# Optimization experiments

Measured on AMD Instinct MI355X. Metric: run time of the kernel, lower is better.

## Reference

```python
import jax, jax.numpy as jnp
import numpy as np

N_NODES = 10000
N_EDGES = 320000
NEG_SLOPE = 0.2
EPS = 1e-12


def _gat_layer(x, W, a_src, a_dst, b, src, dst, n, heads, out_c):
    # x: [n, in_c]; W: [in_c, heads*out_c]; a_src/a_dst: [heads, out_c]; b: [heads*out_c]
    h = (x @ W).reshape(n, heads, out_c)                     # [n, H, C]
    e_src = jnp.einsum('nhc,hc->nh', h, a_src)               # [n, H]
    e_dst = jnp.einsum('nhc,hc->nh', h, a_dst)               # [n, H]
    e = e_src[src] + e_dst[dst]                              # [E, H]
    e = jnp.where(e > 0, e, NEG_SLOPE * e)                   # leaky_relu
    # segment softmax over incoming edges of each destination node
    emax = jax.ops.segment_max(e, dst, num_segments=n)       # [n, H]
    ex = jnp.exp(e - emax[dst])                              # [E, H]
    denom = jax.ops.segment_sum(ex, dst, num_segments=n)     # [n, H]
    alpha = ex / denom[dst]                                  # [E, H]
    out = jax.ops.segment_sum(alpha[:, :, None] * h[src], dst, num_segments=n)
    return out.reshape(n, heads * out_c) + b


def setup_inputs() -> dict:
    key = jax.random.key(0)
    ks = jax.random.split(key, 16)
    n, e = N_NODES, N_EDGES
    x1 = jax.random.normal(ks[0], (n, 10), dtype=jnp.float32)
    x2 = jax.random.normal(ks[1], (n, 10), dtype=jnp.float32)
    edge_index = jax.random.randint(ks[2], (2, e), 0, n, dtype=jnp.int64)
    s = 0.2
    params = {
        'W1': jax.random.normal(ks[3], (10, 32), dtype=jnp.float32) * s,
        'a_src1': jax.random.normal(ks[4], (8, 4), dtype=jnp.float32) * s,
        'a_dst1': jax.random.normal(ks[5], (8, 4), dtype=jnp.float32) * s,
        'b1': jnp.zeros((32,), dtype=jnp.float32),
        'W2': jax.random.normal(ks[6], (32, 16), dtype=jnp.float32) * s,
        'a_src2': jax.random.normal(ks[7], (4, 4), dtype=jnp.float32) * s,
        'a_dst2': jax.random.normal(ks[8], (4, 4), dtype=jnp.float32) * s,
        'b2': jnp.zeros((16,), dtype=jnp.float32),
        'W3': jax.random.normal(ks[9], (16, 8), dtype=jnp.float32) * s,
        'a_src3': jax.random.normal(ks[10], (2, 4), dtype=jnp.float32) * s,
        'a_dst3': jax.random.normal(ks[11], (2, 4), dtype=jnp.float32) * s,
        'b3': jnp.zeros((8,), dtype=jnp.float32),
        'lin2_w': jax.random.normal(ks[12], (8, 1), dtype=jnp.float32) * s,
    }
    return {'x1': x1, 'x2': x2, 'edge_index': edge_index, 'num_nodes': n, **params}


def reference(x1, x2, edge_index, num_nodes, W1, a_src1, a_dst1, b1, W2, a_src2, a_dst2, b2, W3, a_src3, a_dst3, b3, lin2_w):
    n = num_nodes
    row, col = edge_index[0], edge_index[1]
    # dense adjacency with ones on edges, diag filled with 1, then L1 row-normalized
    adj = jnp.zeros((n, n), dtype=x1.dtype).at[row, col].set(1.0)
    diag = jnp.arange(n)
    adj = adj.at[diag, diag].set(1.0)
    adj = adj / jnp.maximum(jnp.sum(jnp.abs(adj), axis=1, keepdims=True), EPS)
    # GATConv adds self-loops internally
    sl = jnp.arange(n, dtype=edge_index.dtype)
    src = jnp.concatenate([row, sl])
    dst = jnp.concatenate([col, sl])
    x3 = jax.nn.relu(_gat_layer(x1, W1, a_src1, a_dst1, b1, src, dst, n, 8, 4))
    x4 = jax.nn.relu(_gat_layer(x3, W2, a_src2, a_dst2, b2, src, dst, n, 4, 4))
    x6 = jax.nn.relu(_gat_layer(x4, W3, a_src3, a_dst3, b3, src, dst, n, 2, 4))
    # eval mode: F.dropout is a no-op
    R = x6 @ x6.T                                            # [n, n]
    R_2 = jnp.sum(R * adj, axis=1, keepdims=True)            # [n, 1]
    local_score = R_2 + x1[:, 0:1]
    global_score = (adj @ x6) @ lin2_w                       # [n, 1]
    return local_score + global_score
```

## Files before the change

### kernel.cpp

```cpp
#include <hip/hip_runtime.h>

#define TPB 256
#define CAP 128
#define POI 0xAAAAAAAAu

__global__ __launch_bounds__(256) void scatter_t1_kernel(
        const int* __restrict__ edge, int E, int n,
        int* __restrict__ fill,  int* __restrict__ csr,
        int* __restrict__ rfill, int* __restrict__ rcsr,
        const float* __restrict__ x, const float* __restrict__ W,
        const float* __restrict__ asrc, const float* __restrict__ adst,
        float* __restrict__ h, float* __restrict__ es, float* __restrict__ ed) {
    constexpr int IN = 10, H = 8, HC = 32;
    __shared__ float sW[IN * HC];
    __shared__ float sa[HC];
    __shared__ float sd[HC];
    for (int i = threadIdx.x; i < IN * HC; i += blockDim.x) sW[i] = W[i];
    if (threadIdx.x < HC) { sa[threadIdx.x] = asrc[threadIdx.x]; sd[threadIdx.x] = adst[threadIdx.x]; }
    __syncthreads();

    int part = blockIdx.x & 7;
    int bi   = blockIdx.x >> 3;
    int Bp   = gridDim.x >> 3;
    const int4* rrow = (const int4*)edge;
    const int4* crow = (const int4*)(edge + E);
    int E4 = E >> 2;
    for (int i = bi * blockDim.x + threadIdx.x; i < E4; i += Bp * blockDim.x) {
        int4 r4 = rrow[i];
        int4 c4 = crow[i];
        int rs[4] = {r4.x, r4.y, r4.z, r4.w};
        int cs[4] = {c4.x, c4.y, c4.z, c4.w};
#pragma unroll
        for (int u = 0; u < 4; u++) {
            int r = rs[u], c = cs[u];
            if ((c & 7) == part) {
                unsigned p = (unsigned)atomicAdd(&fill[c], 1) - POI;
                if (p < CAP) csr[c * CAP + p] = r;
            }
            if ((r & 7) == part) {
                unsigned q = (unsigned)atomicAdd(&rfill[r], 1) - POI;
                if (q < CAP) rcsr[r * CAP + q] = c;
            }
        }
    }

    int gid = blockIdx.x * blockDim.x + threadIdx.x;
    int stride = gridDim.x * blockDim.x;
    for (int tid = gid; tid < n * H; tid += stride) {
        int node = tid / H;
        int hd   = tid % H;
        float xv[IN];
#pragma unroll
        for (int k = 0; k < IN; k++) xv[k] = x[(size_t)node * IN + k];
        float e1 = 0.f, e2 = 0.f;
        float4 hv;
        float* hp = &hv.x;
#pragma unroll
        for (int c = 0; c < 4; c++) {
            int o = hd * 4 + c;
            float acc = 0.f;
#pragma unroll
            for (int k = 0; k < IN; k++) acc += xv[k] * sW[k * HC + o];
            hp[c] = acc;
            e1 += acc * sa[o];
            e2 += acc * sd[o];
        }
        *(float4*)&h[(size_t)node * HC + hd * 4] = hv;
        es[(size_t)node * H + hd] = e1;
        ed[(size_t)node * H + hd] = e2;
    }
}

__device__ __forceinline__ int bucket_len(const int* __restrict__ fill, int node) {
    unsigned v = (unsigned)fill[node] - POI;
    return (v > CAP) ? CAP : (int)v;
}

__global__ __launch_bounds__(256) void agg1_t2_kernel(
        const int* __restrict__ fill, const int* __restrict__ csr,
        const float* __restrict__ h1, const float* __restrict__ es1,
        const float* __restrict__ ed1, const float* __restrict__ b1,
        const float* __restrict__ W2, const float* __restrict__ as2,
        const float* __restrict__ ad2,
        int n, float* __restrict__ h2, float* __restrict__ es2,
        float* __restrict__ ed2) {
    __shared__ float sW2[32 * 16];
    __shared__ float sa2[16], sd2[16], sb1[32];
    for (int i = threadIdx.x; i < 32 * 16; i += blockDim.x) sW2[i] = W2[i];
    if (threadIdx.x < 16) { sa2[threadIdx.x] = as2[threadIdx.x]; sd2[threadIdx.x] = ad2[threadIdx.x]; }
    if (threadIdx.x < 32) sb1[threadIdx.x] = b1[threadIdx.x];
    __syncthreads();

    int half  = threadIdx.x >> 5;
    int slane = threadIdx.x & 31;
    int node  = blockIdx.x * 8 + half;
    if (node >= n) return;
    int len = bucket_len(fill, node);
    int base = node * CAP;

    float edv[8];
#pragma unroll
    for (int hd = 0; hd < 8; hd++) edv[hd] = ed1[(size_t)node * 8 + hd];

    float den[8];
    float4 acc[8];
#pragma unroll
    for (int hd = 0; hd < 8; hd++) { den[hd] = 0.f; acc[hd] = make_float4(0.f, 0.f, 0.f, 0.f); }

    for (int k = slane; k <= len; k += 32) {
        int s = (k < len) ? csr[base + k] : node;
        const float4* esr = (const float4*)&es1[(size_t)s * 8];
        float4 ea = esr[0], eb = esr[1];
        float esrow[8] = {ea.x, ea.y, ea.z, ea.w, eb.x, eb.y, eb.z, eb.w};
        const float4* hr = (const float4*)&h1[(size_t)s * 32];
#pragma unroll
        for (int hd = 0; hd < 8; hd++) {
            float e = esrow[hd] + edv[hd];
            e = (e > 0.f) ? e : 0.2f * e;
            float w = __expf(e);
            float4 hv = hr[hd];
            den[hd]   += w;
            acc[hd].x += w * hv.x;
            acc[hd].y += w * hv.y;
            acc[hd].z += w * hv.z;
            acc[hd].w += w * hv.w;
        }
    }
    for (int off = 16; off > 0; off >>= 1) {
#pragma unroll
        for (int hd = 0; hd < 8; hd++) {
            den[hd]   += __shfl_xor(den[hd],   off, 64);
            acc[hd].x += __shfl_xor(acc[hd].x, off, 64);
            acc[hd].y += __shfl_xor(acc[hd].y, off, 64);
            acc[hd].z += __shfl_xor(acc[hd].z, off, 64);
            acc[hd].w += __shfl_xor(acc[hd].w, off, 64);
        }
    }
    float x3[32];
#pragma unroll
    for (int hd = 0; hd < 8; hd++) {
        float inv = 1.0f / den[hd];
        float v;
        v = acc[hd].x * inv + sb1[hd * 4 + 0]; x3[hd * 4 + 0] = v > 0.f ? v : 0.f;
        v = acc[hd].y * inv + sb1[hd * 4 + 1]; x3[hd * 4 + 1] = v > 0.f ? v : 0.f;
        v = acc[hd].z * inv + sb1[hd * 4 + 2]; x3[hd * 4 + 2] = v > 0.f ? v : 0.f;
        v = acc[hd].w * inv + sb1[hd * 4 + 3]; x3[hd * 4 + 3] = v > 0.f ? v : 0.f;
    }
    if (slane < 16) {
        int o = slane;
        float a = 0.f;
#pragma unroll
        for (int k = 0; k < 32; k++) a += x3[k] * sW2[k * 16 + o];
        h2[(size_t)node * 16 + o] = a;
        float p1 = a * sa2[o];
        float p2 = a * sd2[o];
        p1 += __shfl_xor(p1, 1, 64); p1 += __shfl_xor(p1, 2, 64);
        p2 += __shfl_xor(p2, 1, 64); p2 += __shfl_xor(p2, 2, 64);
        if ((o & 3) == 0) {
            int hd = o >> 2;
            es2[(size_t)node * 4 + hd] = p1;
            ed2[(size_t)node * 4 + hd] = p2;
        }
    }
}

__global__ __launch_bounds__(256) void agg2_t3_kernel(
        const int* __restrict__ fill, const int* __restrict__ csr,
        const float* __restrict__ h2, const float* __restrict__ es2,
        const float* __restrict__ ed2, const float* __restrict__ b2,
        const float* __restrict__ W3, const float* __restrict__ as3,
        const float* __restrict__ ad3,
        int n, float* __restrict__ h3, float* __restrict__ es3,
        float* __restrict__ ed3) {
    __shared__ float sW3[16 * 8];
    __shared__ float sa3[8], sd3[8], sb2[16];
    for (int i = threadIdx.x; i < 16 * 8; i += blockDim.x) sW3[i] = W3[i];
    if (threadIdx.x < 8)  { sa3[threadIdx.x] = as3[threadIdx.x]; sd3[threadIdx.x] = ad3[threadIdx.x]; }
    if (threadIdx.x < 16) sb2[threadIdx.x] = b2[threadIdx.x];
    __syncthreads();

    int half  = threadIdx.x >> 5;
    int slane = threadIdx.x & 31;
    int node  = blockIdx.x * 8 + half;
    if (node >= n) return;
    int len = bucket_len(fill, node);
    int base = node * CAP;

    float edv[4];
#pragma unroll
    for (int hd = 0; hd < 4; hd++) edv[hd] = ed2[(size_t)node * 4 + hd];

    float den[4];
    float4 acc[4];
#pragma unroll
    for (int hd = 0; hd < 4; hd++) { den[hd] = 0.f; acc[hd] = make_float4(0.f, 0.f, 0.f, 0.f); }

    for (int k = slane; k <= len; k += 32) {
        int s = (k < len) ? csr[base + k] : node;
        float4 ea = *(const float4*)&es2[(size_t)s * 4];
        float esrow[4] = {ea.x, ea.y, ea.z, ea.w};
        const float4* hr = (const float4*)&h2[(size_t)s * 16];
#pragma unroll
        for (int hd = 0; hd < 4; hd++) {
            float e = esrow[hd] + edv[hd];
            e = (e > 0.f) ? e : 0.2f * e;
            float w = __expf(e);
            float4 hv = hr[hd];
            den[hd]   += w;
            acc[hd].x += w * hv.x;
            acc[hd].y += w * hv.y;
            acc[hd].z += w * hv.z;
            acc[hd].w += w * hv.w;
        }
    }
    for (int off = 16; off > 0; off >>= 1) {
#pragma unroll
        for (int hd = 0; hd < 4; hd++) {
            den[hd]   += __shfl_xor(den[hd],   off, 64);
            acc[hd].x += __shfl_xor(acc[hd].x, off, 64);
            acc[hd].y += __shfl_xor(acc[hd].y, off, 64);
            acc[hd].z += __shfl_xor(acc[hd].z, off, 64);
            acc[hd].w += __shfl_xor(acc[hd].w, off, 64);
        }
    }
    float x4[16];
#pragma unroll
    for (int hd = 0; hd < 4; hd++) {
        float inv = 1.0f / den[hd];
        float v;
        v = acc[hd].x * inv + sb2[hd * 4 + 0]; x4[hd * 4 + 0] = v > 0.f ? v : 0.f;
        v = acc[hd].y * inv + sb2[hd * 4 + 1]; x4[hd * 4 + 1] = v > 0.f ? v : 0.f;
        v = acc[hd].z * inv + sb2[hd * 4 + 2]; x4[hd * 4 + 2] = v > 0.f ? v : 0.f;
        v = acc[hd].w * inv + sb2[hd * 4 + 3]; x4[hd * 4 + 3] = v > 0.f ? v : 0.f;
    }
    if (slane < 8) {
        int o = slane;
        float a = 0.f;
#pragma unroll
        for (int k = 0; k < 16; k++) a += x4[k] * sW3[k * 8 + o];
        h3[(size_t)node * 8 + o] = a;
        float p1 = a * sa3[o];
        float p2 = a * sd3[o];
        p1 += __shfl_xor(p1, 1, 64); p1 += __shfl_xor(p1, 2, 64);
        p2 += __shfl_xor(p2, 1, 64); p2 += __shfl_xor(p2, 2, 64);
        if ((o & 3) == 0) {
            int hd = o >> 2;
            es3[(size_t)node * 2 + hd] = p1;
            ed3[(size_t)node * 2 + hd] = p2;
        }
    }
}

__global__ __launch_bounds__(256) void aggregate3_kernel(
        const int* __restrict__ fill, const int* __restrict__ csr,
        const float* __restrict__ h, const float* __restrict__ es,
        const float* __restrict__ ed, const float* __restrict__ bias,
        int n, float* __restrict__ xout) {
    int half  = threadIdx.x >> 5;
    int slane = threadIdx.x & 31;
    int node  = blockIdx.x * 8 + half;
    if (node >= n) return;
    int len = bucket_len(fill, node);
    int base = node * CAP;

    float edv[2];
    edv[0] = ed[(size_t)node * 2 + 0];
    edv[1] = ed[(size_t)node * 2 + 1];
    float den[2] = {0.f, 0.f};
    float4 acc[2];
    acc[0] = make_float4(0.f, 0.f, 0.f, 0.f);
    acc[1] = make_float4(0.f, 0.f, 0.f, 0.f);

    for (int k = slane; k <= len; k += 32) {
        int s = (k < len) ? csr[base + k] : node;
        float2 ea = *(const float2*)&es[(size_t)s * 2];
        float esrow[2] = {ea.x, ea.y};
        const float4* hr = (const float4*)&h[(size_t)s * 8];
#pragma unroll
        for (int hd = 0; hd < 2; hd++) {
            float e = esrow[hd] + edv[hd];
            e = (e > 0.f) ? e : 0.2f * e;
            float w = __expf(e);
            float4 hv = hr[hd];
            den[hd]   += w;
            acc[hd].x += w * hv.x;
            acc[hd].y += w * hv.y;
            acc[hd].z += w * hv.z;
            acc[hd].w += w * hv.w;
        }
    }
    for (int off = 16; off > 0; off >>= 1) {
#pragma unroll
        for (int hd = 0; hd < 2; hd++) {
            den[hd]   += __shfl_xor(den[hd],   off, 64);
            acc[hd].x += __shfl_xor(acc[hd].x, off, 64);
            acc[hd].y += __shfl_xor(acc[hd].y, off, 64);
            acc[hd].z += __shfl_xor(acc[hd].z, off, 64);
            acc[hd].w += __shfl_xor(acc[hd].w, off, 64);
        }
    }
    if (slane == 0) {
#pragma unroll
        for (int hd = 0; hd < 2; hd++) {
            float inv = 1.0f / den[hd];
            const float* bp = &bias[hd * 4];
            float4 o;
            float v;
            v = acc[hd].x * inv + bp[0]; o.x = v > 0.f ? v : 0.f;
            v = acc[hd].y * inv + bp[1]; o.y = v > 0.f ? v : 0.f;
            v = acc[hd].z * inv + bp[2]; o.z = v > 0.f ? v : 0.f;
            v = acc[hd].w * inv + bp[3]; o.w = v > 0.f ? v : 0.f;
            *(float4*)&xout[(size_t)node * 8 + hd * 4] = o;
        }
    }
}

__global__ __launch_bounds__(256) void final_kernel(const float* __restrict__ x6,
                             const int* __restrict__ rfill, const int* __restrict__ rcsr,
                             const float* __restrict__ x1, const float* __restrict__ lw,
                             float* __restrict__ out, int n) {
    int wave = threadIdx.x >> 6;
    int lane = threadIdx.x & 63;
    int node = blockIdx.x * 4 + wave;
    if (node >= n) return;
    int d = bucket_len(rfill, node);
    int beg = node * CAP;
    const float4* x6v = (const float4*)x6;
    float4 s0 = make_float4(0.f, 0.f, 0.f, 0.f);
    float4 s1 = make_float4(0.f, 0.f, 0.f, 0.f);
    int ndl = 0;
    bool selfl = false;
    if (d <= 64) {
        int c = (lane < d) ? rcsr[beg + lane] : -1;
        bool dup = false;
        for (int t = 0; t < d - 1; t++) {
            int v = __shfl(c, t, 64);
            dup |= (lane > t) && (c == v);
        }
        if ((lane < d) && !dup) {
            ndl = 1;
            selfl = (c == node);
            s0 = x6v[(size_t)c * 2];
            s1 = x6v[(size_t)c * 2 + 1];
        }
    } else {
        for (int k = beg + lane; k < beg + d; k += 64) {
            int c = rcsr[k];
            bool dup = false;
            for (int j = beg; j < k; j++) if (rcsr[j] == c) { dup = true; break; }
            if (!dup) {
                ndl++;
                selfl |= (c == node);
                float4 a = x6v[(size_t)c * 2];
                float4 b = x6v[(size_t)c * 2 + 1];
                s0.x += a.x; s0.y += a.y; s0.z += a.z; s0.w += a.w;
                s1.x += b.x; s1.y += b.y; s1.z += b.z; s1.w += b.w;
            }
        }
    }
    for (int off = 32; off > 0; off >>= 1) {
        s0.x += __shfl_xor(s0.x, off, 64);
        s0.y += __shfl_xor(s0.y, off, 64);
        s0.z += __shfl_xor(s0.z, off, 64);
        s0.w += __shfl_xor(s0.w, off, 64);
        s1.x += __shfl_xor(s1.x, off, 64);
        s1.y += __shfl_xor(s1.y, off, 64);
        s1.z += __shfl_xor(s1.z, off, 64);
        s1.w += __shfl_xor(s1.w, off, 64);
        ndl  += __shfl_xor(ndl, off, 64);
    }
    bool selfSet = __any(selfl);
    if (lane == 0) {
        float4 me0 = x6v[(size_t)node * 2];
        float4 me1 = x6v[(size_t)node * 2 + 1];
        if (!selfSet) {
            s0.x += me0.x; s0.y += me0.y; s0.z += me0.z; s0.w += me0.w;
            s1.x += me1.x; s1.y += me1.y; s1.z += me1.z; s1.w += me1.w;
            ndl += 1;
        }
        float r2 = s0.x * me0.x + s0.y * me0.y + s0.z * me0.z + s0.w * me0.w
                 + s1.x * me1.x + s1.y * me1.y + s1.z * me1.z + s1.w * me1.w;
        float gs = s0.x * lw[0] + s0.y * lw[1] + s0.z * lw[2] + s0.w * lw[3]
                 + s1.x * lw[4] + s1.y * lw[5] + s1.z * lw[6] + s1.w * lw[7];
        out[node] = (r2 + gs) / (float)ndl + x1[(size_t)node * 10];
    }
}

static inline size_t align16(size_t x) { return (x + 15) & ~(size_t)15; }

extern "C" void kernel_launch(void* const* d_in, const int* in_sizes, int n_in,
                              void* d_out, int out_size, void* d_ws, size_t ws_size,
                              hipStream_t stream) {
    const float* x1  = (const float*)d_in[0];
    const int*   edge = (const int*)d_in[2];
    const float* W1  = (const float*)d_in[4];
    const float* as1 = (const float*)d_in[5];
    const float* ad1 = (const float*)d_in[6];
    const float* b1  = (const float*)d_in[7];
    const float* W2  = (const float*)d_in[8];
    const float* as2 = (const float*)d_in[9];
    const float* ad2 = (const float*)d_in[10];
    const float* b2  = (const float*)d_in[11];
    const float* W3  = (const float*)d_in[12];
    const float* as3 = (const float*)d_in[13];
    const float* ad3 = (const float*)d_in[14];
    const float* b3  = (const float*)d_in[15];
    const float* lw  = (const float*)d_in[16];
    float* out = (float*)d_out;

    const int n = in_sizes[0] / 10;
    const int E = in_sizes[2] / 2;

    char* p = (char*)d_ws;
    int*   fill    = (int*)p;   p += align16((size_t)n * 4);
    int*   rfill   = (int*)p;   p += align16((size_t)n * 4);
    int*   csr     = (int*)p;   p += align16((size_t)n * CAP * 4);
    int*   rcsr    = (int*)p;   p += align16((size_t)n * CAP * 4);
    float* h1  = (float*)p; p += align16((size_t)n * 32 * 4);
    float* es1 = (float*)p; p += align16((size_t)n * 8 * 4);
    float* ed1 = (float*)p; p += align16((size_t)n * 8 * 4);
    float* h2  = (float*)p; p += align16((size_t)n * 16 * 4);
    float* es2 = (float*)p; p += align16((size_t)n * 4 * 4);
    float* ed2 = (float*)p; p += align16((size_t)n * 4 * 4);
    float* h3  = (float*)p; p += align16((size_t)n * 8 * 4);
    float* es3 = (float*)p; p += align16((size_t)n * 2 * 4);
    float* ed3 = (float*)p; p += align16((size_t)n * 2 * 4);
    float* x6  = (float*)p; p += align16((size_t)n * 8 * 4);


    scatter_t1_kernel<<<1024, TPB, 0, stream>>>(
        edge, E, n, fill, csr, rfill, rcsr, x1, W1, as1, ad1, h1, es1, ed1);

    agg1_t2_kernel<<<(n + 7) / 8, TPB, 0, stream>>>(
        fill, csr, h1, es1, ed1, b1, W2, as2, ad2, n, h2, es2, ed2);

    agg2_t3_kernel<<<(n + 7) / 8, TPB, 0, stream>>>(
        fill, csr, h2, es2, ed2, b2, W3, as3, ad3, n, h3, es3, ed3);

    aggregate3_kernel<<<(n + 7) / 8, TPB, 0, stream>>>(
        fill, csr, h3, es3, ed3, b3, n, x6);

    final_kernel<<<(n + 3) / 4, 256, 0, stream>>>(x6, rfill, rcsr, x1, lw, out, n);
}
```

Measured before the change: 172.3 us.

## Split heads across half-groups in GAT aggregation and batch scatter atomics

In the three aggregation kernels, each 32-lane group now splits into two 16-lane halves that each handle half of the heads, with lanes striding over edges by 16 instead of 32. This cuts per-thread register arrays and shuffle-reduction work and adds a cross-half shuffle to finish the following linear layer. The edge scatter kernel now issues all fill and rfill atomics for its four edges before doing any CSR stores, so atomic latencies can overlap. The risk is less edge-level parallelism per node, since each lane now walks twice as many edges.

Measured after the change: 169.4 us. About the same (-1.7%).

```diff
diff --git a/kernel.cpp b/kernel.cpp
--- a/kernel.cpp
+++ b/kernel.cpp
@@ -30,18 +30,25 @@
         int4 c4 = crow[i];
         int rs[4] = {r4.x, r4.y, r4.z, r4.w};
         int cs[4] = {c4.x, c4.y, c4.z, c4.w};
+        unsigned ps[4] = {~0u, ~0u, ~0u, ~0u};
+        unsigned qs[4] = {~0u, ~0u, ~0u, ~0u};
+        bool pc[4], qc[4];
 #pragma unroll
         for (int u = 0; u < 4; u++) {
-            int r = rs[u], c = cs[u];
-            if ((c & 7) == part) {
-                unsigned p = (unsigned)atomicAdd(&fill[c], 1) - POI;
-                if (p < CAP) csr[c * CAP + p] = r;
-            }
-            if ((r & 7) == part) {
-                unsigned q = (unsigned)atomicAdd(&rfill[r], 1) - POI;
-                if (q < CAP) rcsr[r * CAP + q] = c;
-            }
-        }
+            pc[u] = ((cs[u] & 7) == part);
+            if (pc[u]) ps[u] = (unsigned)atomicAdd(&fill[cs[u]], 1) - POI;
+        }
+#pragma unroll
+        for (int u = 0; u < 4; u++) {
+            qc[u] = ((rs[u] & 7) == part);
+            if (qc[u]) qs[u] = (unsigned)atomicAdd(&rfill[rs[u]], 1) - POI;
+        }
+#pragma unroll
+        for (int u = 0; u < 4; u++)
+            if (pc[u] && ps[u] < CAP) csr[cs[u] * CAP + ps[u]] = rs[u];
+#pragma unroll
+        for (int u = 0; u < 4; u++)
+            if (qc[u] && qs[u] < CAP) rcsr[rs[u] * CAP + qs[u]] = cs[u];
     }
 
     int gid = blockIdx.x * blockDim.x + threadIdx.x;
@@ -93,29 +100,30 @@
 
     int half  = threadIdx.x >> 5;
     int slane = threadIdx.x & 31;
+    int sub   = slane >> 4;
+    int j     = slane & 15;
     int node  = blockIdx.x * 8 + half;
     if (node >= n) return;
     int len = bucket_len(fill, node);
     int base = node * CAP;
 
-    float edv[8];
-#pragma unroll
-    for (int hd = 0; hd < 8; hd++) edv[hd] = ed1[(size_t)node * 8 + hd];
-
-    float den[8];
-    float4 acc[8];
-#pragma unroll
-    for (int hd = 0; hd < 8; hd++) { den[hd] = 0.f; acc[hd] = make_float4(0.f, 0.f, 0.f, 0.f); }
-
-    for (int k = slane; k <= len; k += 32) {
+    float edv[4];
+#pragma unroll
+    for (int hd = 0; hd < 4; hd++) edv[hd] = ed1[(size_t)node * 8 + sub * 4 + hd];
+
+    float den[4];
+    float4 acc[4];
+#pragma unroll
+    for (int hd = 0; hd < 4; hd++) { den[hd] = 0.f; acc[hd] = make_float4(0.f, 0.f, 0.f, 0.f); }
+
+    for (int k = j; k <= len; k += 16) {
         int s = (k < len) ? csr[base + k] : node;
-        const float4* esr = (const float4*)&es1[(size_t)s * 8];
-        float4 ea = esr[0], eb = esr[1];
-        float esrow[8] = {ea.x, ea.y, ea.z, ea.w, eb.x, eb.y, eb.z, eb.w};
-        const float4* hr = (const float4*)&h1[(size_t)s * 32];
-#pragma unroll
-        for (int hd = 0; hd < 8; hd++) {
-            float e = esrow[hd] + edv[hd];
+        float4 ea = *(const float4*)&es1[(size_t)s * 8 + sub * 4];
+        float er[4] = {ea.x, ea.y, ea.z, ea.w};
+        const float4* hr = (const float4*)&h1[(size_t)s * 32 + sub * 16];
+#pragma unroll
+        for (int hd = 0; hd < 4; hd++) {
+            float e = er[hd] + edv[hd];
             e = (e > 0.f) ? e : 0.2f * e;
             float w = __expf(e);
             float4 hv = hr[hd];
@@ -126,9 +134,9 @@
             acc[hd].w += w * hv.w;
         }
     }
-    for (int off = 16; off > 0; off >>= 1) {
-#pragma unroll
-        for (int hd = 0; hd < 8; hd++) {
+    for (int off = 8; off > 0; off >>= 1) {
+#pragma unroll
+        for (int hd = 0; hd < 4; hd++) {
             den[hd]   += __shfl_xor(den[hd],   off, 64);
             acc[hd].x += __shfl_xor(acc[hd].x, off, 64);
             acc[hd].y += __shfl_xor(acc[hd].y, off, 64);
@@ -136,21 +144,23 @@
             acc[hd].w += __shfl_xor(acc[hd].w, off, 64);
         }
     }
-    float x3[32];
-#pragma unroll
-    for (int hd = 0; hd < 8; hd++) {
+    float x3h[16];
+#pragma unroll
+    for (int hd = 0; hd < 4; hd++) {
         float inv = 1.0f / den[hd];
+        int c0 = sub * 16 + hd * 4;
         float v;
-        v = acc[hd].x * inv + sb1[hd * 4 + 0]; x3[hd * 4 + 0] = v > 0.f ? v : 0.f;
-        v = acc[hd].y * inv + sb1[hd * 4 + 1]; x3[hd * 4 + 1] = v > 0.f ? v : 0.f;
-        v = acc[hd].z * inv + sb1[hd * 4 + 2]; x3[hd * 4 + 2] = v > 0.f ? v : 0.f;
-        v = acc[hd].w * inv + sb1[hd * 4 + 3]; x3[hd * 4 + 3] = v > 0.f ? v : 0.f;
-    }
-    if (slane < 16) {
-        int o = slane;
-        float a = 0.f;
-#pragma unroll
-        for (int k = 0; k < 32; k++) a += x3[k] * sW2[k * 16 + o];
+        v = acc[hd].x * inv + sb1[c0 + 0]; x3h[hd * 4 + 0] = v > 0.f ? v : 0.f;
+        v = acc[hd].y * inv + sb1[c0 + 1]; x3h[hd * 4 + 1] = v > 0.f ? v : 0.f;
+        v = acc[hd].z * inv + sb1[c0 + 2]; x3h[hd * 4 + 2] = v > 0.f ? v : 0.f;
+        v = acc[hd].w * inv + sb1[c0 + 3]; x3h[hd * 4 + 3] = v > 0.f ? v : 0.f;
+    }
+    int o = j;
+    float a = 0.f;
+#pragma unroll
+    for (int k2 = 0; k2 < 16; k2++) a += x3h[k2] * sW2[(sub * 16 + k2) * 16 + o];
+    a += __shfl_xor(a, 16, 64);
+    if (sub == 0) {
         h2[(size_t)node * 16 + o] = a;
         float p1 = a * sa2[o];
         float p2 = a * sd2[o];
@@ -181,28 +191,30 @@
 
     int half  = threadIdx.x >> 5;
     int slane = threadIdx.x & 31;
+    int sub   = slane >> 4;
+    int j     = slane & 15;
     int node  = blockIdx.x * 8 + half;
     if (node >= n) return;
     int len = bucket_len(fill, node);
     int base = node * CAP;
 
-    float edv[4];
-#pragma unroll
-    for (int hd = 0; hd < 4; hd++) edv[hd] = ed2[(size_t)node * 4 + hd];
-
-    float den[4];
-    float4 acc[4];
-#pragma unroll
-    for (int hd = 0; hd < 4; hd++) { den[hd] = 0.f; acc[hd] = make_float4(0.f, 0.f, 0.f, 0.f); }
-
-    for (int k = slane; k <= len; k += 32) {
+    float edv[2];
+#pragma unroll
+    for (int hd = 0; hd < 2; hd++) edv[hd] = ed2[(size_t)node * 4 + sub * 2 + hd];
+
+    float den[2];
+    float4 acc[2];
+#pragma unroll
+    for (int hd = 0; hd < 2; hd++) { den[hd] = 0.f; acc[hd] = make_float4(0.f, 0.f, 0.f, 0.f); }
+
+    for (int k = j; k <= len; k += 16) {
         int s = (k < len) ? csr[base + k] : node;
-        float4 ea = *(const float4*)&es2[(size_t)s * 4];
-        float esrow[4] = {ea.x, ea.y, ea.z, ea.w};
-        const float4* hr = (const float4*)&h2[(size_t)s * 16];
-#pragma unroll
-        for (int hd = 0; hd < 4; hd++) {
-            float e = esrow[hd] + edv[hd];
+        float2 ea = *(const float2*)&es2[(size_t)s * 4 + sub * 2];
+        float er[2] = {ea.x, ea.y};
+        const float4* hr = (const float4*)&h2[(size_t)s * 16 + sub * 8];
+#pragma unroll
+        for (int hd = 0; hd < 2; hd++) {
+            float e = er[hd] + edv[hd];
             e = (e > 0.f) ? e : 0.2f * e;
             float w = __expf(e);
             float4 hv = hr[hd];
@@ -213,9 +225,9 @@
             acc[hd].w += w * hv.w;
         }
     }
-    for (int off = 16; off > 0; off >>= 1) {
-#pragma unroll
-        for (int hd = 0; hd < 4; hd++) {
+    for (int off = 8; off > 0; off >>= 1) {
+#pragma unroll
+        for (int hd = 0; hd < 2; hd++) {
             den[hd]   += __shfl_xor(den[hd],   off, 64);
             acc[hd].x += __shfl_xor(acc[hd].x, off, 64);
             acc[hd].y += __shfl_xor(acc[hd].y, off, 64);
@@ -223,30 +235,34 @@
             acc[hd].w += __shfl_xor(acc[hd].w, off, 64);
         }
     }
-    float x4[16];
-#pragma unroll
-    for (int hd = 0; hd < 4; hd++) {
+    float x4h[8];
+#pragma unroll
+    for (int hd = 0; hd < 2; hd++) {
         float inv = 1.0f / den[hd];
+        int c0 = sub * 8 + hd * 4;
         float v;
-        v = acc[hd].x * inv + sb2[hd * 4 + 0]; x4[hd * 4 + 0] = v > 0.f ? v : 0.f;
-        v = acc[hd].y * inv + sb2[hd * 4 + 1]; x4[hd * 4 + 1] = v > 0.f ? v : 0.f;
-        v = acc[hd].z * inv + sb2[hd * 4 + 2]; x4[hd * 4 + 2] = v > 0.f ? v : 0.f;
-        v = acc[hd].w * inv + sb2[hd * 4 + 3]; x4[hd * 4 + 3] = v > 0.f ? v : 0.f;
-    }
-    if (slane < 8) {
-        int o = slane;
+        v = acc[hd].x * inv + sb2[c0 + 0]; x4h[hd * 4 + 0] = v > 0.f ? v : 0.f;
+        v = acc[hd].y * inv + sb2[c0 + 1]; x4h[hd * 4 + 1] = v > 0.f ? v : 0.f;
+        v = acc[hd].z * inv + sb2[c0 + 2]; x4h[hd * 4 + 2] = v > 0.f ? v : 0.f;
+        v = acc[hd].w * inv + sb2[c0 + 3]; x4h[hd * 4 + 3] = v > 0.f ? v : 0.f;
+    }
+    if (j < 8) {
+        int o = j;
         float a = 0.f;
 #pragma unroll
-        for (int k = 0; k < 16; k++) a += x4[k] * sW3[k * 8 + o];
-        h3[(size_t)node * 8 + o] = a;
-        float p1 = a * sa3[o];
-        float p2 = a * sd3[o];
-        p1 += __shfl_xor(p1, 1, 64); p1 += __shfl_xor(p1, 2, 64);
-        p2 += __shfl_xor(p2, 1, 64); p2 += __shfl_xor(p2, 2, 64);
-        if ((o & 3) == 0) {
-            int hd = o >> 2;
-            es3[(size_t)node * 2 + hd] = p1;
-            ed3[(size_t)node * 2 + hd] = p2;
+        for (int k2 = 0; k2 < 8; k2++) a += x4h[k2] * sW3[(sub * 8 + k2) * 8 + o];
+        a += __shfl_xor(a, 16, 64);
+        if (sub == 0) {
+            h3[(size_t)node * 8 + o] = a;
+            float p1 = a * sa3[o];
+            float p2 = a * sd3[o];
+            p1 += __shfl_xor(p1, 1, 64); p1 += __shfl_xor(p1, 2, 64);
+            p2 += __shfl_xor(p2, 1, 64); p2 += __shfl_xor(p2, 2, 64);
+            if ((o & 3) == 0) {
+                int hd = o >> 2;
+                es3[(size_t)node * 2 + hd] = p1;
+                ed3[(size_t)node * 2 + hd] = p2;
+            }
         }
     }
 }
@@ -258,60 +274,46 @@
         int n, float* __restrict__ xout) {
     int half  = threadIdx.x >> 5;
     int slane = threadIdx.x & 31;
+    int sub   = slane >> 4;
+    int j     = slane & 15;
     int node  = blockIdx.x * 8 + half;
     if (node >= n) return;
     int len = bucket_len(fill, node);
     int base = node * CAP;
 
-    float edv[2];
-    edv[0] = ed[(size_t)node * 2 + 0];
-    edv[1] = ed[(size_t)node * 2 + 1];
-    float den[2] = {0.f, 0.f};
-    float4 acc[2];
-    acc[0] = make_float4(0.f, 0.f, 0.f, 0.f);
-    acc[1] = make_float4(0.f, 0.f, 0.f, 0.f);
-
-    for (int k = slane; k <= len; k += 32) {
+    float edv = ed[(size_t)node * 2 + sub];
+    float den = 0.f;
+    float4 acc = make_float4(0.f, 0.f, 0.f, 0.f);
+
+    for (int k = j; k <= len; k += 16) {
         int s = (k < len) ? csr[base + k] : node;
-        float2 ea = *(const float2*)&es[(size_t)s * 2];
-        float esrow[2] = {ea.x, ea.y};
-        const float4* hr = (const float4*)&h[(size_t)s * 8];
-#pragma unroll
-        for (int hd = 0; hd < 2; hd++) {
-            float e = esrow[hd] + edv[hd];
-            e = (e > 0.f) ? e : 0.2f * e;
-            float w = __expf(e);
-            float4 hv = hr[hd];
-            den[hd]   += w;
-            acc[hd].x += w * hv.x;
-            acc[hd].y += w * hv.y;
-            acc[hd].z += w * hv.z;
-            acc[hd].w += w * hv.w;
-        }
-    }
-    for (int off = 16; off > 0; off >>= 1) {
-#pragma unroll
-        for (int hd = 0; hd < 2; hd++) {
-            den[hd]   += __shfl_xor(den[hd],   off, 64);
-            acc[hd].x += __shfl_xor(acc[hd].x, off, 64);
-            acc[hd].y += __shfl_xor(acc[hd].y, off, 64);
-            acc[hd].z += __shfl_xor(acc[hd].z, off, 64);
-            acc[hd].w += __shfl_xor(acc[hd].w, off, 64);
-        }
-    }
-    if (slane == 0) {
-#pragma unroll
-        for (int hd = 0; hd < 2; hd++) {
-            float inv = 1.0f / den[hd];
-            const float* bp = &bias[hd * 4];
-            float4 o;
-            float v;
-            v = acc[hd].x * inv + bp[0]; o.x = v > 0.f ? v : 0.f;
-            v = acc[hd].y * inv + bp[1]; o.y = v > 0.f ? v : 0.f;
-            v = acc[hd].z * inv + bp[2]; o.z = v > 0.f ? v : 0.f;
-            v = acc[hd].w * inv + bp[3]; o.w = v > 0.f ? v : 0.f;
-            *(float4*)&xout[(size_t)node * 8 + hd * 4] = o;
-        }
+        float e = es[(size_t)s * 2 + sub] + edv;
+        e = (e > 0.f) ? e : 0.2f * e;
+        float w = __expf(e);
+        float4 hv = *(const float4*)&h[(size_t)s * 8 + sub * 4];
+        den   += w;
+        acc.x += w * hv.x;
+        acc.y += w * hv.y;
+        acc.z += w * hv.z;
+        acc.w += w * hv.w;
+    }
+    for (int off = 8; off > 0; off >>= 1) {
+        den   += __shfl_xor(den,   off, 64);
+        acc.x += __shfl_xor(acc.x, off, 64);
+        acc.y += __shfl_xor(acc.y, off, 64);
+        acc.z += __shfl_xor(acc.z, off, 64);
+        acc.w += __shfl_xor(acc.w, off, 64);
+    }
+    if (j == 0) {
+        float inv = 1.0f / den;
+        const float* bp = &bias[sub * 4];
+        float4 o;
+        float v;
+        v = acc.x * inv + bp[0]; o.x = v > 0.f ? v : 0.f;
+        v = acc.y * inv + bp[1]; o.y = v > 0.f ? v : 0.f;
+        v = acc.z * inv + bp[2]; o.z = v > 0.f ? v : 0.f;
+        v = acc.w * inv + bp[3]; o.w = v > 0.f ? v : 0.f;
+        *(float4*)&xout[(size_t)node * 8 + sub * 4] = o;
     }
 }
 
```
